# Kernel tuning notes

Hardware: AMD Instinct MI355X
Metric: run time of the kernel (lower is better)

Reference implementation:

```python
import jax, jax.numpy as jnp
import numpy as np

E, T, H, I = 64, 2048, 512, 1024


def setup_inputs() -> dict:
    key = jax.random.key(0)
    k1, k2, k3 = jax.random.split(key, 3)
    x = jax.random.normal(k1, (T, E, H), dtype=jnp.float32)
    # trunc_normal_(std=sqrt(0.1/fan_in)) approximated by normal with same std
    wi = jax.random.normal(k2, (E, H, I), dtype=jnp.float32) * (0.1 / H) ** 0.5
    wo = jax.random.normal(k3, (E, I, H), dtype=jnp.float32) * (0.1 / I) ** 0.5
    return {"x": x, "wi": wi, "wo": wo}


def reference(x, wi, wo):
    # x: [T, E, H] -> transpose to [E, T, H] (reshape(e,-1,h) is a no-op for 3D input)
    xt = jnp.transpose(x, (1, 0, 2))
    # expert GEMM 1 + exact GELU (torch nn.GELU default is erf-based)
    h = jax.nn.gelu(jnp.einsum('eth,ehi->eti', xt, wi), approximate=False)
    # dropout is skipped when expert_parallel is None; grad scalers are identity (ep_size=1)
    out = jnp.einsum('eti,eih->eth', h, wo)
    return jnp.transpose(out, (1, 0, 2))  # back to [T, E, H]
```

## Files before the change

### kernel.cpp

```cpp
#include <hip/hip_runtime.h>
#include <stdint.h>

#define NE 64
#define NT 2048
#define NH 512
#define NI 1024

typedef __attribute__((ext_vector_type(8))) short bf16x8;
typedef __attribute__((ext_vector_type(4))) float f32x4;
typedef __attribute__((ext_vector_type(16))) float f32x16;

typedef const __attribute__((address_space(1))) void* gptr1_t;
typedef __attribute__((address_space(3))) void* lptr3_t;
#define GLOAD16(g, l) \
  __builtin_amdgcn_global_load_lds((gptr1_t)(const void*)(g), (lptr3_t)(void*)(l), 16, 0, 0)

static __device__ __forceinline__ uint16_t f2bf(float f) {
  uint32_t u = __builtin_bit_cast(uint32_t, f);
  u += 0x7fffu + ((u >> 16) & 1u);
  return (uint16_t)(u >> 16);
}

static __device__ __forceinline__ float gelu_erf(float v) {
  return 0.5f * v * (1.0f + erff(v * 0.7071067811865475f));
}

__global__ __launch_bounds__(256)
void cast_x(const float* __restrict__ x, uint16_t* __restrict__ xB,
            int t_start, int S) {
  const int total = S * NE * (NH / 8);
  for (int c = blockIdx.x * 256 + threadIdx.x; c < total; c += gridDim.x * 256) {
    const int hb = c & 63;
    const int e = (c >> 6) & 63;
    const int t = c >> 12;
    const float* ip = x + ((size_t)(t_start + t) * NE + e) * NH + (hb << 3);
    const f32x4 v0 = *(const f32x4*)ip;
    const f32x4 v1 = *(const f32x4*)(ip + 4);
    bf16x8 w;
#pragma unroll
    for (int u = 0; u < 4; ++u) {
      w[u] = (short)f2bf(v0[u]);
      w[u + 4] = (short)f2bf(v1[u]);
    }
    *(bf16x8*)&xB[((size_t)e * S + t) * NH + (hb << 3)] = w;
  }
}

__global__ __launch_bounds__(256)
void conv_tr(const float* __restrict__ in, uint16_t* __restrict__ out, int K, int N) {
  const int e = blockIdx.x;
  const int k0 = blockIdx.y << 6;
  const int n0 = blockIdx.z << 6;
  __shared__ uint16_t t[64][72];
  const int tid = threadIdx.x;
  const int r = tid >> 2;
  const int c0 = (tid & 3) << 4;
  const float* ip = in + ((size_t)e * K + k0 + r) * N + n0 + c0;
#pragma unroll
  for (int j = 0; j < 16; j += 4) {
    f32x4 v = *(const f32x4*)(ip + j);
#pragma unroll
    for (int u = 0; u < 4; ++u) t[c0 + j + u][r] = f2bf(v[u]);
  }
  __syncthreads();
  uint16_t* op = out + ((size_t)e * N + n0 + r) * K + k0 + c0;
  *(bf16x8*)op = *(const bf16x8*)&t[r][c0];
  *(bf16x8*)(op + 8) = *(const bf16x8*)&t[r][c0 + 8];
}

__global__ __launch_bounds__(256, 4)
void k_gemm1(const uint16_t* __restrict__ xB, const uint16_t* __restrict__ wiB,
             uint16_t* __restrict__ h, int Ts) {
  const int Mt = Ts >> 7;
  const int nwg = gridDim.x;
  const int wid = (blockIdx.x & 7) * (nwg >> 3) + (blockIdx.x >> 3);
  const int bn = wid & 7;
  const int bm = (wid >> 3) % Mt;
  const int be = wid / (Mt << 3);
  const int t0 = bm << 7, n0 = bn << 7;

  __shared__ __align__(16) uint16_t As[8192];
  __shared__ __align__(16) uint16_t Bs[8192];

  const int tid = threadIdx.x, lane = tid & 63;
  const int wy = (tid >> 7) & 1, wx = (tid >> 6) & 1;

  const uint16_t* Abase = xB + ((size_t)be * Ts + t0) * NH;
  const uint16_t* Bbase = wiB + ((size_t)be * NI + n0) * NH;

  int off[4], ldsOff[4];
#pragma unroll
  for (int s = 0; s < 4; ++s) {
    const int c = (s << 8) + tid;
    const int rr = c >> 3, kgs = c & 7;
    off[s] = (rr << 9) + ((kgs ^ (rr & 7)) << 3);
    ldsOff[s] = c << 4;
  }

  f32x4 acc[4][4];
#pragma unroll
  for (int i = 0; i < 4; ++i)
#pragma unroll
    for (int j = 0; j < 4; ++j) acc[i][j] = (f32x4){0.f, 0.f, 0.f, 0.f};

  const int KIT = NH >> 6;
  for (int it = 0; it < KIT; ++it) {
    __syncthreads();
#pragma unroll
    for (int s = 0; s < 4; ++s)
      GLOAD16(Abase + (it << 6) + off[s], (char*)As + ldsOff[s]);
#pragma unroll
    for (int s = 0; s < 4; ++s)
      GLOAD16(Bbase + (it << 6) + off[s], (char*)Bs + ldsOff[s]);
    __syncthreads();
#pragma unroll
    for (int ks = 0; ks < 2; ++ks) {
      const int kg = (ks << 2) + (lane >> 4);
      bf16x8 af[4], bfr[4];
#pragma unroll
      for (int mi = 0; mi < 4; ++mi) {
        const int row = (wy << 6) + (mi << 4) + (lane & 15);
        af[mi] = *(const bf16x8*)&As[(row << 6) + ((kg ^ (row & 7)) << 3)];
      }
#pragma unroll
      for (int ni = 0; ni < 4; ++ni) {
        const int col = (wx << 6) + (ni << 4) + (lane & 15);
        bfr[ni] = *(const bf16x8*)&Bs[(col << 6) + ((kg ^ (col & 7)) << 3)];
      }
#pragma unroll
      for (int mi = 0; mi < 4; ++mi)
#pragma unroll
        for (int ni = 0; ni < 4; ++ni)
          acc[mi][ni] = __builtin_amdgcn_mfma_f32_16x16x32_bf16(
              af[mi], bfr[ni], acc[mi][ni], 0, 0, 0);
    }
  }

#pragma unroll
  for (int mi = 0; mi < 4; ++mi) {
#pragma unroll
    for (int ni = 0; ni < 4; ++ni) {
      const int col = n0 + (wx << 6) + (ni << 4) + (lane & 15);
#pragma unroll
      for (int j = 0; j < 4; ++j) {
        const int r = t0 + (wy << 6) + (mi << 4) + ((lane >> 4) << 2) + j;
        h[((size_t)be * Ts + r) * NI + col] = f2bf(gelu_erf(acc[mi][ni][j]));
      }
    }
  }
}

__global__ __launch_bounds__(256, 4)
void k_gemm2(const uint16_t* __restrict__ hA, const uint16_t* __restrict__ woB,
             float* __restrict__ out, int t_start, int Ts) {
  const int Mt = Ts >> 7;
  const int nwg = gridDim.x;
  const int wid = (blockIdx.x & 7) * (nwg >> 3) + (blockIdx.x >> 3);
  const int bn = wid & 3;
  const int bm = (wid >> 2) % Mt;
  const int be = wid / (Mt << 2);
  const int t0 = bm << 7, n0 = bn << 7;

  __shared__ __align__(16) uint16_t As[8192];
  __shared__ __align__(16) uint16_t Bs[8192];

  const int tid = threadIdx.x, lane = tid & 63;
  const int wy = (tid >> 7) & 1, wx = (tid >> 6) & 1;
  const int l31 = lane & 31, l5 = lane >> 5;

  const uint16_t* Abase = hA + ((size_t)be * Ts + t0) * NI;
  const uint16_t* Bbase = woB + ((size_t)be * NH + n0) * NI;

  int off[4], ldsOff[4];
#pragma unroll
  for (int s = 0; s < 4; ++s) {
    const int c = (s << 8) + tid;
    const int rr = c >> 3, kgs = c & 7;
    off[s] = (rr << 10) + ((kgs ^ (rr & 7)) << 3);
    ldsOff[s] = c << 4;
  }

  f32x16 acc[2][2];
#pragma unroll
  for (int i = 0; i < 2; ++i)
#pragma unroll
    for (int j = 0; j < 2; ++j)
#pragma unroll
      for (int u = 0; u < 16; ++u) acc[i][j][u] = 0.f;

  const int KIT = NI >> 6;
  for (int it = 0; it < KIT; ++it) {
    __syncthreads();
#pragma unroll
    for (int s = 0; s < 4; ++s)
      GLOAD16(Abase + (it << 6) + off[s], (char*)As + ldsOff[s]);
#pragma unroll
    for (int s = 0; s < 4; ++s)
      GLOAD16(Bbase + (it << 6) + off[s], (char*)Bs + ldsOff[s]);
    __syncthreads();
#pragma unroll
    for (int ks = 0; ks < 4; ++ks) {
      const int kg = (ks << 1) + l5;
      bf16x8 af[2], bfr[2];
#pragma unroll
      for (int mi = 0; mi < 2; ++mi) {
        const int row = (wy << 6) + (mi << 5) + l31;
        af[mi] = *(const bf16x8*)&As[(row << 6) + ((kg ^ (row & 7)) << 3)];
      }
#pragma unroll
      for (int ni = 0; ni < 2; ++ni) {
        const int col = (wx << 6) + (ni << 5) + l31;
        bfr[ni] = *(const bf16x8*)&Bs[(col << 6) + ((kg ^ (col & 7)) << 3)];
      }
#pragma unroll
      for (int mi = 0; mi < 2; ++mi)
#pragma unroll
        for (int ni = 0; ni < 2; ++ni)
          acc[mi][ni] = __builtin_amdgcn_mfma_f32_32x32x16_bf16(
              af[mi], bfr[ni], acc[mi][ni], 0, 0, 0);
    }
  }

#pragma unroll
  for (int mi = 0; mi < 2; ++mi) {
#pragma unroll
    for (int ni = 0; ni < 2; ++ni) {
      const int col = n0 + (wx << 6) + (ni << 5) + l31;
#pragma unroll
      for (int g = 0; g < 4; ++g) {
#pragma unroll
        for (int j = 0; j < 4; ++j) {
          const int row = t0 + (wy << 6) + (mi << 5) + (g << 3) + (l5 << 2) + j;
          out[((size_t)(t_start + row) * NE + be) * NH + col] =
              acc[mi][ni][(g << 2) + j];
        }
      }
    }
  }
}

extern "C" void kernel_launch(void* const* d_in, const int* in_sizes, int n_in,
                              void* d_out, int out_size, void* d_ws, size_t ws_size,
                              hipStream_t stream) {
  const float* x = (const float*)d_in[0];
  const float* wi = (const float*)d_in[1];
  const float* wo = (const float*)d_in[2];
  float* out = (float*)d_out;

  uint16_t* wiB = (uint16_t*)d_ws;
  uint16_t* woB = (uint16_t*)((char*)d_ws + 67108864);
  char* rest = (char*)d_ws + 134217728;

  const size_t perRow = (size_t)NE * NH * 2 + (size_t)NE * NI * 2;
  size_t avail = (ws_size > 134217728u) ? ws_size - 134217728u : 0;
  int Ts = (int)(avail / perRow);
  Ts &= ~127;
  if (Ts > NT) Ts = NT;
  if (Ts < 128) Ts = 128;

  hipLaunchKernelGGL(conv_tr, dim3(NE, NH / 64, NI / 64), dim3(256), 0, stream,
                     wi, wiB, NH, NI);
  hipLaunchKernelGGL(conv_tr, dim3(NE, NI / 64, NH / 64), dim3(256), 0, stream,
                     wo, woB, NI, NH);

  for (int ts = 0; ts < NT; ts += Ts) {
    int cur = NT - ts;
    if (cur > Ts) cur = Ts;
    const int Mt = cur >> 7;
    uint16_t* xB = (uint16_t*)rest;
    uint16_t* h = (uint16_t*)(rest + (size_t)NE * cur * NH * 2);
    const int castGrid = (cur * NE * (NH / 8) + 255) / 256;
    hipLaunchKernelGGL(cast_x, dim3(castGrid < 2048 ? castGrid : 2048), dim3(256),
                       0, stream, x, xB, ts, cur);
    hipLaunchKernelGGL(k_gemm1, dim3(Mt * 8 * NE), dim3(256), 0, stream,
                       xB, wiB, h, cur);
    hipLaunchKernelGGL(k_gemm2, dim3(Mt * 4 * NE), dim3(256), 0, stream,
                       h, woB, out, ts, cur);
  }
}
```

Measured before the change: 572.9 us.

## Fuse x fp32-to-bf16 cast into GEMM1 A-tile load and merge weight conversions

Removes the separate cast_x kernel. GEMM1 now loads fp32 x directly from global memory into registers, prefetching the next k-tile, then converts to bf16 and writes the swizzled LDS tile. The two weight transpose-convert launches become one combined launch, and the T chunk size is capped at 512 so the bf16 h buffer stays small and likely cache-resident. The cost is that each x row is read and converted 8 times, once per N-tile, instead of once, and the A path now goes through registers rather than direct-to-LDS loads. More chunk iterations also add launch overhead.

```diff
diff --git a/kernel.cpp b/kernel.cpp
--- a/kernel.cpp
+++ b/kernel.cpp
@@ -26,31 +26,26 @@
 }
 
 __global__ __launch_bounds__(256)
-void cast_x(const float* __restrict__ x, uint16_t* __restrict__ xB,
-            int t_start, int S) {
-  const int total = S * NE * (NH / 8);
-  for (int c = blockIdx.x * 256 + threadIdx.x; c < total; c += gridDim.x * 256) {
-    const int hb = c & 63;
-    const int e = (c >> 6) & 63;
-    const int t = c >> 12;
-    const float* ip = x + ((size_t)(t_start + t) * NE + e) * NH + (hb << 3);
-    const f32x4 v0 = *(const f32x4*)ip;
-    const f32x4 v1 = *(const f32x4*)(ip + 4);
-    bf16x8 w;
-#pragma unroll
-    for (int u = 0; u < 4; ++u) {
-      w[u] = (short)f2bf(v0[u]);
-      w[u + 4] = (short)f2bf(v1[u]);
-    }
-    *(bf16x8*)&xB[((size_t)e * S + t) * NH + (hb << 3)] = w;
-  }
-}
-
-__global__ __launch_bounds__(256)
-void conv_tr(const float* __restrict__ in, uint16_t* __restrict__ out, int K, int N) {
-  const int e = blockIdx.x;
-  const int k0 = blockIdx.y << 6;
-  const int n0 = blockIdx.z << 6;
+void conv_both(const float* __restrict__ wi, const float* __restrict__ wo,
+               uint16_t* __restrict__ wiB, uint16_t* __restrict__ woB) {
+  int id = blockIdx.x;
+  const float* in;
+  uint16_t* out;
+  int K, N, k0, n0, e;
+  if (id < NE * 128) {
+    e = id >> 7;
+    const int rem = id & 127;
+    k0 = (rem >> 4) << 6;
+    n0 = (rem & 15) << 6;
+    in = wi; out = wiB; K = NH; N = NI;
+  } else {
+    id -= NE * 128;
+    e = id >> 7;
+    const int rem = id & 127;
+    k0 = (rem >> 3) << 6;
+    n0 = (rem & 7) << 6;
+    in = wo; out = woB; K = NI; N = NH;
+  }
   __shared__ uint16_t t[64][72];
   const int tid = threadIdx.x;
   const int r = tid >> 2;
@@ -69,8 +64,8 @@
 }
 
 __global__ __launch_bounds__(256, 4)
-void k_gemm1(const uint16_t* __restrict__ xB, const uint16_t* __restrict__ wiB,
-             uint16_t* __restrict__ h, int Ts) {
+void k_gemm1(const float* __restrict__ x, const uint16_t* __restrict__ wiB,
+             uint16_t* __restrict__ h, int t_start, int Ts) {
   const int Mt = Ts >> 7;
   const int nwg = gridDim.x;
   const int wid = (blockIdx.x & 7) * (nwg >> 3) + (blockIdx.x >> 3);
@@ -85,34 +80,57 @@
   const int tid = threadIdx.x, lane = tid & 63;
   const int wy = (tid >> 7) & 1, wx = (tid >> 6) & 1;
 
-  const uint16_t* Abase = xB + ((size_t)be * Ts + t0) * NH;
   const uint16_t* Bbase = wiB + ((size_t)be * NI + n0) * NH;
 
-  int off[4], ldsOff[4];
+  int boff[4], ldsOff[4], aLds[4];
+  const float* aP[4];
 #pragma unroll
   for (int s = 0; s < 4; ++s) {
     const int c = (s << 8) + tid;
     const int rr = c >> 3, kgs = c & 7;
-    off[s] = (rr << 9) + ((kgs ^ (rr & 7)) << 3);
+    boff[s] = rr * NH + ((kgs ^ (rr & 7)) << 3);
     ldsOff[s] = c << 4;
-  }
-
+    aP[s] = x + ((size_t)(t_start + t0 + rr) * NE + be) * NH + (kgs << 3);
+    aLds[s] = (rr << 6) + ((kgs ^ (rr & 7)) << 3);
+  }
+
+  f32x4 ar[4][2];
   f32x4 acc[4][4];
 #pragma unroll
   for (int i = 0; i < 4; ++i)
 #pragma unroll
     for (int j = 0; j < 4; ++j) acc[i][j] = (f32x4){0.f, 0.f, 0.f, 0.f};
 
+  auto loadA = [&](int it) {
+#pragma unroll
+    for (int s = 0; s < 4; ++s) {
+      ar[s][0] = *(const f32x4*)(aP[s] + (it << 6));
+      ar[s][1] = *(const f32x4*)(aP[s] + (it << 6) + 4);
+    }
+  };
+  auto writeA = [&]() {
+#pragma unroll
+    for (int s = 0; s < 4; ++s) {
+      bf16x8 w;
+#pragma unroll
+      for (int u = 0; u < 4; ++u) {
+        w[u] = (short)f2bf(ar[s][0][u]);
+        w[u + 4] = (short)f2bf(ar[s][1][u]);
+      }
+      *(bf16x8*)&As[aLds[s]] = w;
+    }
+  };
+
+  loadA(0);
   const int KIT = NH >> 6;
   for (int it = 0; it < KIT; ++it) {
     __syncthreads();
+    writeA();
 #pragma unroll
     for (int s = 0; s < 4; ++s)
-      GLOAD16(Abase + (it << 6) + off[s], (char*)As + ldsOff[s]);
-#pragma unroll
-    for (int s = 0; s < 4; ++s)
-      GLOAD16(Bbase + (it << 6) + off[s], (char*)Bs + ldsOff[s]);
-    __syncthreads();
+      GLOAD16(Bbase + (it << 6) + boff[s], (char*)Bs + ldsOff[s]);
+    __syncthreads();
+    if (it + 1 < KIT) loadA(it + 1);
 #pragma unroll
     for (int ks = 0; ks < 2; ++ks) {
       const int kg = (ks << 2) + (lane >> 4);
@@ -249,31 +267,24 @@
 
   uint16_t* wiB = (uint16_t*)d_ws;
   uint16_t* woB = (uint16_t*)((char*)d_ws + 67108864);
-  char* rest = (char*)d_ws + 134217728;
-
-  const size_t perRow = (size_t)NE * NH * 2 + (size_t)NE * NI * 2;
+  uint16_t* h = (uint16_t*)((char*)d_ws + 134217728);
+
+  const size_t perRow = (size_t)NE * NI * 2;
   size_t avail = (ws_size > 134217728u) ? ws_size - 134217728u : 0;
   int Ts = (int)(avail / perRow);
+  if (Ts > 512) Ts = 512;
   Ts &= ~127;
-  if (Ts > NT) Ts = NT;
   if (Ts < 128) Ts = 128;
 
-  hipLaunchKernelGGL(conv_tr, dim3(NE, NH / 64, NI / 64), dim3(256), 0, stream,
-                     wi, wiB, NH, NI);
-  hipLaunchKernelGGL(conv_tr, dim3(NE, NI / 64, NH / 64), dim3(256), 0, stream,
-                     wo, woB, NI, NH);
+  hipLaunchKernelGGL(conv_both, dim3(2 * NE * 128), dim3(256), 0, stream,
+                     wi, wo, wiB, woB);
 
   for (int ts = 0; ts < NT; ts += Ts) {
     int cur = NT - ts;
     if (cur > Ts) cur = Ts;
     const int Mt = cur >> 7;
-    uint16_t* xB = (uint16_t*)rest;
-    uint16_t* h = (uint16_t*)(rest + (size_t)NE * cur * NH * 2);
-    const int castGrid = (cur * NE * (NH / 8) + 255) / 256;
-    hipLaunchKernelGGL(cast_x, dim3(castGrid < 2048 ? castGrid : 2048), dim3(256),
-                       0, stream, x, xB, ts, cur);
     hipLaunchKernelGGL(k_gemm1, dim3(Mt * 8 * NE), dim3(256), 0, stream,
-                       xB, wiB, h, cur);
+                       x, wiB, h, ts, cur);
     hipLaunchKernelGGL(k_gemm2, dim3(Mt * 4 * NE), dim3(256), 0, stream,
                        h, woB, out, ts, cur);
   }
```

Measured after the change: 658.7 us. 1.15x slower.
